# Kernel optimization log

Hardware: AMD Instinct MI355X
Metric: run time of the kernel (lower is better)

## Reference

```python
import jax, jax.numpy as jnp
import numpy as np

B, T, H = 1024, 512, 256  # batch, seq_len, hidden_layer_size; input_size=1, output_size=1


def setup_inputs() -> dict:
    key = jax.random.key(0)
    ks = jax.random.split(key, 7)
    s = 1.0 / np.sqrt(H)  # PyTorch LSTM/Linear init scale (uniform bound); normal here, scaled similarly
    return {
        "input_seq": jax.random.normal(ks[0], (B, T), dtype=jnp.float32),
        "W_ih": jax.random.normal(ks[1], (4 * H, 1), dtype=jnp.float32) * s,
        "W_hh": jax.random.normal(ks[2], (4 * H, H), dtype=jnp.float32) * s,
        "b_ih": jax.random.normal(ks[3], (4 * H,), dtype=jnp.float32) * s,
        "b_hh": jax.random.normal(ks[4], (4 * H,), dtype=jnp.float32) * s,
        "W_lin": jax.random.normal(ks[5], (1, H), dtype=jnp.float32) * s,
        "b_lin": jax.random.normal(ks[6], (1,), dtype=jnp.float32) * s,
    }


def _lstm_last_hidden(x, W_ih, W_hh, b_ih, b_hh):
    # x: [B, T] scalar series -> treated as [B, T, 1] (input_size = 1).
    # Precompute the input projection for all timesteps at once:
    # xg[b, t, :] = x[b, t] * W_ih[:, 0] + b_ih + b_hh   -> [B, T, 4H]
    xg = x[:, :, None] * W_ih[:, 0] + (b_ih + b_hh)
    xg = jnp.swapaxes(xg, 0, 1)  # [T, B, 4H] for scan over time

    h0 = jnp.zeros((x.shape[0], H), dtype=x.dtype)
    c0 = jnp.zeros((x.shape[0], H), dtype=x.dtype)

    def step(carry, xg_t):
        h, c = carry
        gates = xg_t + h @ W_hh.T  # [B, 4H]
        i, f, g, o = jnp.split(gates, 4, axis=-1)  # PyTorch gate order: i, f, g, o
        i = jax.nn.sigmoid(i)
        f = jax.nn.sigmoid(f)
        g = jnp.tanh(g)
        o = jax.nn.sigmoid(o)
        c = f * c + i * g
        h = o * jnp.tanh(c)
        return (h, c), None

    (h_n, _), _ = jax.lax.scan(step, (h0, c0), xg)
    return h_n  # [B, H]


def reference(input_seq, W_ih, W_hh, b_ih, b_hh, W_lin, b_lin):
    h_n = _lstm_last_hidden(input_seq, W_ih, W_hh, b_ih, b_hh)
    predictions = h_n @ W_lin.T + b_lin  # [B, 1]
    return predictions
```

## Files before the change

kernel.cpp:

```cpp
#include <hip/hip_runtime.h>


#define HID 256
#define TT 512
#define BROWS 16
#define NBLK 64
#define THREADS 512

typedef float v4f __attribute__((ext_vector_type(4)));
typedef unsigned int v4u __attribute__((ext_vector_type(4)));
typedef __bf16 v8bf __attribute__((ext_vector_type(8)));

__device__ __forceinline__ unsigned short f2bf(float f) {
    unsigned int u = __builtin_bit_cast(unsigned int, f);
    u += 0x7fffu + ((u >> 16) & 1u);
    return (unsigned short)(u >> 16);
}
__device__ __forceinline__ float bf2f(unsigned short s) {
    unsigned int u = ((unsigned int)s) << 16;
    return __builtin_bit_cast(float, u);
}
__device__ __forceinline__ float fsigmoid(float x) {
    float e = exp2f(x * -1.44269504f);
    return __builtin_amdgcn_rcpf(1.0f + e);
}
__device__ __forceinline__ float ftanh(float x) {
    float e = exp2f(x * 2.88539008f);
    return 1.0f - 2.0f * __builtin_amdgcn_rcpf(1.0f + e);
}

__global__ void wconv_kernel(const float* __restrict__ Whh,
                             unsigned short* __restrict__ Wbf) {
    int tid = blockIdx.x * blockDim.x + threadIdx.x;
    int lane = tid & 63;
    int frag = tid >> 6;
    int Tn = frag >> 3;
    int kc = frag & 7;
    int n  = Tn * 16 + (lane & 15);
    int kb = kc * 32 + (lane >> 4) * 8;
    const float* src = Whh + (size_t)n * HID + kb;
    unsigned short* dst = Wbf + (size_t)tid * 8;
#pragma unroll
    for (int j = 0; j < 8; ++j) dst[j] = f2bf(src[j]);
}

#define MFMA8(ACC, BARR, BOFF)                                               \
    _Pragma("unroll")                                                        \
    for (int kc = 0; kc < 8; ++kc)                                           \
        ACC = __builtin_amdgcn_mfma_f32_16x16x32_bf16(afrag[kc],             \
                  BARR[(BOFF) + kc], ACC, 0, 0, 0);

#define LDSTILE(ACC, SLOT)                                                   \
    { v8bf bl_[8];                                                           \
      _Pragma("unroll")                                                      \
      for (int kc = 0; kc < 8; ++kc)                                         \
          bl_[kc] = __builtin_bit_cast(v8bf, *(const v4u*)(Wlds +            \
                      ((size_t)(((SLOT) * 8 + kc) * 64 + lane)) * 8));       \
      MFMA8(ACC, bl_, 0) }

#define SLOADT(SB, TN)                                                       \
    _Pragma("unroll")                                                        \
    for (int kc = 0; kc < 8; ++kc)                                           \
        SB[kc] = __builtin_bit_cast(v8bf,                                    \
                   Wv[((size_t)(TN) * 8 + kc) * 64 + lane]);

#define INITG(S, AI, AF, AG, AO)                                             \
    { int nb = 16 * (w + 8 * (S)) + l4;                                      \
      float w0 = gw[nb],       b0 = gb[nb];                                  \
      float w1 = gw[256 + nb], b1 = gb[256 + nb];                            \
      float w2 = gw[512 + nb], b2 = gb[512 + nb];                            \
      float w3 = gw[768 + nb], b3 = gb[768 + nb];                            \
      _Pragma("unroll")                                                      \
      for (int r = 0; r < 4; ++r) {                                          \
          AI[r] = xv[r] * w0 + b0; AF[r] = xv[r] * w1 + b1;                  \
          AG[r] = xv[r] * w2 + b2; AO[r] = xv[r] * w3 + b3; } }

#define GATES(S, AI, AF, AG, AO)                                             \
    { int n_ = 16 * (w + 8 * (S)) + l4;                                      \
      int gn = n_ >> 3;                                                      \
      _Pragma("unroll")                                                      \
      for (int r = 0; r < 4; ++r) {                                          \
        float gi = fsigmoid(AI[r]);                                          \
        float gf = fsigmoid(AF[r]);                                          \
        float gg = ftanh(AG[r]);                                             \
        float go = fsigmoid(AO[r]);                                          \
        float cn = gf * c_st[(S) * 4 + r] + gi * gg;                         \
        c_st[(S) * 4 + r] = cn;                                              \
        int m = quad * 4 + r;                                                \
        hn_[m * 256 + ((gn ^ m) & 31) * 8 + (n_ & 7)] = f2bf(go * ftanh(cn));\
      } }

__global__ __launch_bounds__(THREADS, 2)
void lstm_kernel(const float* __restrict__ x,
                 const float* __restrict__ W_ih,
                 const float* __restrict__ b_ih,
                 const float* __restrict__ b_hh,
                 const float* __restrict__ W_lin,
                 const float* __restrict__ b_lin,
                 const unsigned short* __restrict__ Wbf,
                 float* __restrict__ out) {
    __shared__ __align__(16) unsigned short Wlds[16 * 8 * 64 * 8];
    __shared__ __align__(16) unsigned short hbuf[2][BROWS * 256];
    __shared__ float gw[1024];
    __shared__ float gb[1024];
    __shared__ float part[THREADS];

    const int tid  = threadIdx.x;
    const int lane = tid & 63;
    const int w    = tid >> 6;
    const int l4   = lane & 15;
    const int quad = lane >> 4;
    const int r0   = blockIdx.x * BROWS;

    for (int i = tid; i < 1024; i += THREADS) {
        gw[i] = W_ih[i];
        gb[i] = b_ih[i] + b_hh[i];
    }
    for (int i = tid; i < BROWS * 256; i += THREADS) {
        hbuf[0][i] = 0;
        hbuf[1][i] = 0;
    }

    const v4u* __restrict__ Wv = (const v4u*)Wbf;

    v8bf wres[32];
    {
        const int tns[4] = {w, 16 + w, 8 + w, 24 + w};
#pragma unroll
        for (int qq = 0; qq < 4; ++qq)
#pragma unroll
            for (int kc = 0; kc < 8; ++kc)
                wres[qq * 8 + kc] = __builtin_bit_cast(v8bf,
                    Wv[((size_t)(tns[qq]) * 8 + kc) * 64 + lane]);
    }
#pragma unroll
    for (int S = 0; S < 2; ++S) {
        int Tn = 32 + w + 8 * S;
        int slot = w * 2 + S;
#pragma unroll
        for (int kc = 0; kc < 8; ++kc) {
            v4u d = Wv[((size_t)Tn * 8 + kc) * 64 + lane];
            *(v4u*)(Wlds + ((size_t)((slot * 8 + kc) * 64 + lane)) * 8) = d;
        }
    }
    __syncthreads();

    float c_st[8];
#pragma unroll
    for (int i = 0; i < 8; ++i) c_st[i] = 0.0f;

    v8bf sb[8];
    SLOADT(sb, 48 + w)

    v4f xv;
#pragma unroll
    for (int r = 0; r < 4; ++r)
        xv[r] = x[(size_t)(r0 + quad * 4 + r) * TT];

    int cur = 0;
    for (int t = 0; t < TT; ++t) {
        const unsigned short* hb = hbuf[cur];
        unsigned short* hn_ = hbuf[cur ^ 1];

        v8bf afrag[8];
#pragma unroll
        for (int kc = 0; kc < 8; ++kc)
            afrag[kc] = __builtin_bit_cast(v8bf, *(const v4u*)(
                hb + l4 * 256 + (((kc * 4 + quad) ^ l4) & 31) * 8));

        {
            v4f ai, af2, ag, ao;
            INITG(0, ai, af2, ag, ao)
            MFMA8(ao, sb, 0)
            SLOADT(sb, 56 + w)
            MFMA8(ai, wres, 0)
            MFMA8(af2, wres, 8)
            LDSTILE(ag, w * 2 + 0)
            GATES(0, ai, af2, ag, ao)
        }
        {
            v4f ai, af2, ag, ao;
            INITG(1, ai, af2, ag, ao)
            {
                int tn = (t + 1 < TT) ? (t + 1) : t;
#pragma unroll
                for (int r = 0; r < 4; ++r)
                    xv[r] = x[(size_t)(r0 + quad * 4 + r) * TT + tn];
            }
            MFMA8(ao, sb, 0)
            SLOADT(sb, 48 + w)
            MFMA8(ai, wres, 16)
            MFMA8(af2, wres, 24)
            LDSTILE(ag, w * 2 + 1)
            GATES(1, ai, af2, ag, ao)
        }

        asm volatile("s_waitcnt lgkmcnt(0)\n\ts_barrier" ::: "memory");
        cur ^= 1;
    }

    {
        int rrow = tid >> 5, s5 = tid & 31;
        int pos = (s5 ^ rrow) & 31;
        float p = 0.0f;
#pragma unroll
        for (int jj = 0; jj < 8; ++jj) {
            int j = s5 * 8 + jj;
            p += bf2f(hbuf[cur][rrow * 256 + pos * 8 + jj]) * W_lin[j];
        }
        part[tid] = p;
    }
    __syncthreads();
    if (tid < 16) {
        float sum = 0.0f;
#pragma unroll
        for (int s = 0; s < 32; ++s) sum += part[tid * 32 + s];
        out[r0 + tid] = sum + b_lin[0];
    }
}

extern "C" void kernel_launch(void* const* d_in, const int* in_sizes, int n_in,
                              void* d_out, int out_size, void* d_ws, size_t ws_size,
                              hipStream_t stream) {
    const float* x     = (const float*)d_in[0];
    const float* W_ih  = (const float*)d_in[1];
    const float* W_hh  = (const float*)d_in[2];
    const float* b_ih  = (const float*)d_in[3];
    const float* b_hh  = (const float*)d_in[4];
    const float* W_lin = (const float*)d_in[5];
    const float* b_lin = (const float*)d_in[6];
    unsigned short* Wbf = (unsigned short*)d_ws;

    wconv_kernel<<<128, 256, 0, stream>>>(W_hh, Wbf);
    lstm_kernel<<<NBLK, THREADS, 0, stream>>>(x, W_ih, b_ih, b_hh, W_lin, b_lin,
                                              Wbf, (float*)d_out);
}
```

Before: 1.837 ms.

## Spread batch over 256 blocks of 4 rows and exchange gates via LDS

Each block now processes 4 batch rows instead of 16, so the grid grows from 64 to 256 blocks and covers more compute units. The MFMA tiles still use 16 rows, so rows are duplicated and much of each tile is redundant work. Gate pre-activations are staged through a shared-memory exchange buffer so every lane applies the elementwise LSTM update to only two elements instead of eight. In exchange, each timestep gains an extra LDS round trip and a full __syncthreads, and every block must reload the recurrent weights into its own registers and LDS.

Result: slower. 2.552 ms (+39.0%).

```diff
diff --git a/kernel.cpp b/kernel.cpp
--- a/kernel.cpp
+++ b/kernel.cpp
@@ -3,9 +3,9 @@
 
 #define HID 256
 #define TT 512
-#define BROWS 16
-#define NBLK 64
+#define NBLK 256
 #define THREADS 512
+#define HP 272
 
 typedef float v4f __attribute__((ext_vector_type(4)));
 typedef unsigned int v4u __attribute__((ext_vector_type(4)));
@@ -64,32 +64,6 @@
         SB[kc] = __builtin_bit_cast(v8bf,                                    \
                    Wv[((size_t)(TN) * 8 + kc) * 64 + lane]);
 
-#define INITG(S, AI, AF, AG, AO)                                             \
-    { int nb = 16 * (w + 8 * (S)) + l4;                                      \
-      float w0 = gw[nb],       b0 = gb[nb];                                  \
-      float w1 = gw[256 + nb], b1 = gb[256 + nb];                            \
-      float w2 = gw[512 + nb], b2 = gb[512 + nb];                            \
-      float w3 = gw[768 + nb], b3 = gb[768 + nb];                            \
-      _Pragma("unroll")                                                      \
-      for (int r = 0; r < 4; ++r) {                                          \
-          AI[r] = xv[r] * w0 + b0; AF[r] = xv[r] * w1 + b1;                  \
-          AG[r] = xv[r] * w2 + b2; AO[r] = xv[r] * w3 + b3; } }
-
-#define GATES(S, AI, AF, AG, AO)                                             \
-    { int n_ = 16 * (w + 8 * (S)) + l4;                                      \
-      int gn = n_ >> 3;                                                      \
-      _Pragma("unroll")                                                      \
-      for (int r = 0; r < 4; ++r) {                                          \
-        float gi = fsigmoid(AI[r]);                                          \
-        float gf = fsigmoid(AF[r]);                                          \
-        float gg = ftanh(AG[r]);                                             \
-        float go = fsigmoid(AO[r]);                                          \
-        float cn = gf * c_st[(S) * 4 + r] + gi * gg;                         \
-        c_st[(S) * 4 + r] = cn;                                              \
-        int m = quad * 4 + r;                                                \
-        hn_[m * 256 + ((gn ^ m) & 31) * 8 + (n_ & 7)] = f2bf(go * ftanh(cn));\
-      } }
-
 __global__ __launch_bounds__(THREADS, 2)
 void lstm_kernel(const float* __restrict__ x,
                  const float* __restrict__ W_ih,
@@ -100,28 +74,30 @@
                  const unsigned short* __restrict__ Wbf,
                  float* __restrict__ out) {
     __shared__ __align__(16) unsigned short Wlds[16 * 8 * 64 * 8];
-    __shared__ __align__(16) unsigned short hbuf[2][BROWS * 256];
-    __shared__ float gw[1024];
-    __shared__ float gb[1024];
+    __shared__ __align__(16) unsigned short hbuf[2][4 * HP];
+    __shared__ __align__(16) float xchg[8][2][4][16][4];
     __shared__ float part[THREADS];
+    __shared__ float p2[64];
 
     const int tid  = threadIdx.x;
     const int lane = tid & 63;
     const int w    = tid >> 6;
     const int l4   = lane & 15;
     const int quad = lane >> 4;
-    const int r0   = blockIdx.x * BROWS;
-
-    for (int i = tid; i < 1024; i += THREADS) {
-        gw[i] = W_ih[i];
-        gb[i] = b_ih[i] + b_hh[i];
-    }
-    for (int i = tid; i < BROWS * 256; i += THREADS) {
-        hbuf[0][i] = 0;
-        hbuf[1][i] = 0;
-    }
+    const int r0   = blockIdx.x * 4;
 
     const v4u* __restrict__ Wv = (const v4u*)Wbf;
+
+    float wi[8], bb[8];
+#pragma unroll
+    for (int S = 0; S < 2; ++S) {
+        int u = 16 * (w + 8 * S) + l4;
+#pragma unroll
+        for (int G = 0; G < 4; ++G) {
+            wi[S * 4 + G] = W_ih[G * 256 + u];
+            bb[S * 4 + G] = b_ih[G * 256 + u] + b_hh[G * 256 + u];
+        }
+    }
 
     v8bf wres[32];
     {
@@ -143,79 +119,113 @@
             *(v4u*)(Wlds + ((size_t)((slot * 8 + kc) * 64 + lane)) * 8) = d;
         }
     }
+    for (int i = tid; i < 4 * HP; i += THREADS) {
+        hbuf[0][i] = 0;
+        hbuf[1][i] = 0;
+    }
     __syncthreads();
-
-    float c_st[8];
-#pragma unroll
-    for (int i = 0; i < 8; ++i) c_st[i] = 0.0f;
 
     v8bf sb[8];
     SLOADT(sb, 48 + w)
 
-    v4f xv;
-#pragma unroll
-    for (int r = 0; r < 4; ++r)
-        xv[r] = x[(size_t)(r0 + quad * 4 + r) * TT];
-
-    int cur = 0;
+    float cst[2] = {0.0f, 0.0f};
+
+    float xv[4];
+#pragma unroll
+    for (int r = 0; r < 4; ++r) xv[r] = x[(size_t)(r0 + r) * TT];
+
     for (int t = 0; t < TT; ++t) {
-        const unsigned short* hb = hbuf[cur];
-        unsigned short* hn_ = hbuf[cur ^ 1];
+        const unsigned short* hb = hbuf[t & 1];
+        unsigned short* hn = hbuf[(t & 1) ^ 1];
 
         v8bf afrag[8];
+        const unsigned short* hrow = hb + (l4 & 3) * HP + quad * 8;
 #pragma unroll
         for (int kc = 0; kc < 8; ++kc)
-            afrag[kc] = __builtin_bit_cast(v8bf, *(const v4u*)(
-                hb + l4 * 256 + (((kc * 4 + quad) ^ l4) & 31) * 8));
+            afrag[kc] = __builtin_bit_cast(v8bf, *(const v4u*)(hrow + kc * 32));
 
         {
             v4f ai, af2, ag, ao;
-            INITG(0, ai, af2, ag, ao)
+#pragma unroll
+            for (int r = 0; r < 4; ++r) {
+                ai[r]  = xv[r] * wi[0] + bb[0];
+                af2[r] = xv[r] * wi[1] + bb[1];
+                ag[r]  = xv[r] * wi[2] + bb[2];
+                ao[r]  = xv[r] * wi[3] + bb[3];
+            }
             MFMA8(ao, sb, 0)
             SLOADT(sb, 56 + w)
             MFMA8(ai, wres, 0)
             MFMA8(af2, wres, 8)
             LDSTILE(ag, w * 2 + 0)
-            GATES(0, ai, af2, ag, ao)
+            if (quad == 0) {
+                *(v4f*)&xchg[w][0][0][l4][0] = ai;
+                *(v4f*)&xchg[w][0][1][l4][0] = af2;
+                *(v4f*)&xchg[w][0][2][l4][0] = ag;
+                *(v4f*)&xchg[w][0][3][l4][0] = ao;
+            }
         }
         {
             v4f ai, af2, ag, ao;
-            INITG(1, ai, af2, ag, ao)
+#pragma unroll
+            for (int r = 0; r < 4; ++r) {
+                ai[r]  = xv[r] * wi[4] + bb[4];
+                af2[r] = xv[r] * wi[5] + bb[5];
+                ag[r]  = xv[r] * wi[6] + bb[6];
+                ao[r]  = xv[r] * wi[7] + bb[7];
+            }
             {
                 int tn = (t + 1 < TT) ? (t + 1) : t;
 #pragma unroll
                 for (int r = 0; r < 4; ++r)
-                    xv[r] = x[(size_t)(r0 + quad * 4 + r) * TT + tn];
+                    xv[r] = x[(size_t)(r0 + r) * TT + tn];
             }
             MFMA8(ao, sb, 0)
             SLOADT(sb, 48 + w)
             MFMA8(ai, wres, 16)
             MFMA8(af2, wres, 24)
             LDSTILE(ag, w * 2 + 1)
-            GATES(1, ai, af2, ag, ao)
-        }
-
-        asm volatile("s_waitcnt lgkmcnt(0)\n\ts_barrier" ::: "memory");
-        cur ^= 1;
+            if (quad == 0) {
+                *(v4f*)&xchg[w][1][0][l4][0] = ai;
+                *(v4f*)&xchg[w][1][1][l4][0] = af2;
+                *(v4f*)&xchg[w][1][2][l4][0] = ag;
+                *(v4f*)&xchg[w][1][3][l4][0] = ao;
+            }
+        }
+
+#pragma unroll
+        for (int S = 0; S < 2; ++S) {
+            float gi = fsigmoid(xchg[w][S][0][l4][quad]);
+            float gf = fsigmoid(xchg[w][S][1][l4][quad]);
+            float gg = ftanh   (xchg[w][S][2][l4][quad]);
+            float go = fsigmoid(xchg[w][S][3][l4][quad]);
+            float cn = gf * cst[S] + gi * gg;
+            cst[S] = cn;
+            hn[quad * HP + 16 * (w + 8 * S) + l4] = f2bf(go * ftanh(cn));
+        }
+
+        __syncthreads();
     }
 
     {
-        int rrow = tid >> 5, s5 = tid & 31;
-        int pos = (s5 ^ rrow) & 31;
-        float p = 0.0f;
-#pragma unroll
-        for (int jj = 0; jj < 8; ++jj) {
-            int j = s5 * 8 + jj;
-            p += bf2f(hbuf[cur][rrow * 256 + pos * 8 + jj]) * W_lin[j];
-        }
+        int row = tid >> 7, j0 = (tid & 127) * 2;
+        float p = bf2f(hbuf[0][row * HP + j0]) * W_lin[j0]
+                + bf2f(hbuf[0][row * HP + j0 + 1]) * W_lin[j0 + 1];
         part[tid] = p;
     }
     __syncthreads();
-    if (tid < 16) {
-        float sum = 0.0f;
-#pragma unroll
-        for (int s = 0; s < 32; ++s) sum += part[tid * 32 + s];
-        out[r0 + tid] = sum + b_lin[0];
+    if (tid < 64) {
+        float s = 0.0f;
+#pragma unroll
+        for (int k = 0; k < 8; ++k) s += part[tid * 8 + k];
+        p2[tid] = s;
+    }
+    __syncthreads();
+    if (tid < 4) {
+        float s = 0.0f;
+#pragma unroll
+        for (int k = 0; k < 16; ++k) s += p2[tid * 16 + k];
+        out[r0 + tid] = s + b_lin[0];
     }
 }
 
```
